# Optimization experiments

Hardware: AMD Instinct MI355X
Metric: run time of the kernel (lower is better)

Reference implementation:

```python
import jax, jax.numpy as jnp
import numpy as np

B, T, D, H = 2, 2048, 1024, 16
HD = D // H  # head_size = 64
EPS = 1e-5


def _layernorm(x, g, b):
    mu = jnp.mean(x, axis=-1, keepdims=True)
    var = jnp.mean(jnp.square(x - mu), axis=-1, keepdims=True)
    return (x - mu) * jax.lax.rsqrt(var + EPS) * g + b


def setup_inputs() -> dict:
    key = jax.random.key(0)
    ks = jax.random.split(key, 16)
    s = 0.02
    return {
        "x": jax.random.normal(ks[0], (B, T, D), jnp.float32),
        # per-head Q/K/V linears, stacked over heads: [H, D, HD] (in,out layout)
        "wq": jax.random.normal(ks[1], (H, D, HD), jnp.float32) * s,
        "bq": jnp.zeros((H, HD), jnp.float32),
        "wk": jax.random.normal(ks[2], (H, D, HD), jnp.float32) * s,
        "bk": jnp.zeros((H, HD), jnp.float32),
        "wv": jax.random.normal(ks[3], (H, D, HD), jnp.float32) * s,
        "bv": jnp.zeros((H, HD), jnp.float32),
        "wp": jax.random.normal(ks[4], (D, D), jnp.float32) * s,
        "bp": jnp.zeros((D,), jnp.float32),
        "w1": jax.random.normal(ks[5], (D, 4 * D), jnp.float32) * s,
        "b1": jnp.zeros((4 * D,), jnp.float32),
        "w2": jax.random.normal(ks[6], (4 * D, D), jnp.float32) * s,
        "b2": jnp.zeros((D,), jnp.float32),
        "ln1_g": jnp.ones((D,), jnp.float32),
        "ln1_b": jnp.zeros((D,), jnp.float32),
        "lnf_g": jnp.ones((D,), jnp.float32),
        "lnf_b": jnp.zeros((D,), jnp.float32),
        "ln2_g": jnp.ones((D,), jnp.float32),
        "ln2_b": jnp.zeros((D,), jnp.float32),
    }


def reference(x, wq, bq, wk, bk, wv, bv, wp, bp, w1, b1, w2, b2,
              ln1_g, ln1_b, lnf_g, lnf_b, ln2_g, ln2_b):
    b_, t_, d_ = x.shape
    # batched per-head projections: [B,H,T,HD]
    Q = jnp.einsum('btd,hde->bhte', x, wq) + bq[None, :, None, :]
    K = jnp.einsum('btd,hde->bhte', x, wk) + bk[None, :, None, :]
    V = jnp.einsum('btd,hde->bhte', x, wv) + bv[None, :, None, :]
    # raw attention scores, scaled -- NOTE: no softmax, no mask (matches source)
    wei = jnp.einsum('bhte,bhse->bhts', Q, K) * (HD ** -0.5)
    attn = jnp.einsum('bhts,bhse->bhte', wei, V)  # [B,H,T,HD]
    # concat heads along last dim == [B,T,H*HD]
    cat = attn.transpose(0, 2, 1, 3).reshape(b_, t_, d_)
    Kc = K.transpose(0, 2, 1, 3).reshape(b_, t_, d_)
    Vc = V.transpose(0, 2, 1, 3).reshape(b_, t_, d_)
    out = cat @ wp + bp
    out1 = _layernorm(x + out, ln1_g, ln1_b)
    # FeedForward: ln(idx + net(idx)) internally
    ff = jax.nn.relu(out1 @ w1 + b1) @ w2 + b2
    ffo = _layernorm(out1 + ff, lnf_g, lnf_b)
    out2 = _layernorm(out1 + ffo, ln2_g, ln2_b)
    return (out2, Kc, Vc)
```

## Files before the change

### kernel.cpp

```cpp
#include <hip/hip_runtime.h>

typedef unsigned short u16;
typedef __attribute__((ext_vector_type(4))) float f32x4;
typedef __attribute__((ext_vector_type(8))) __bf16 bf16x8;
typedef __attribute__((ext_vector_type(8))) unsigned short u16x8;
typedef __attribute__((ext_vector_type(4))) unsigned short u16x4;

__device__ __forceinline__ u16 f2b(float f) {
    unsigned int u = __builtin_bit_cast(unsigned int, f);
    u = (u + 0x7FFFu + ((u >> 16) & 1u)) >> 16;
    return (u16)u;
}
__device__ __forceinline__ float b2f(u16 h) {
    unsigned int u = ((unsigned int)h) << 16;
    return __builtin_bit_cast(float, u);
}

__device__ __forceinline__ void gload_lds16(const u16* g, u16* l) {
    __builtin_amdgcn_global_load_lds(
        (const __attribute__((address_space(1))) void*)g,
        (__attribute__((address_space(3))) void*)l,
        16, 0, 0);
}

__device__ __forceinline__ bf16x8 lds_frag(const u16* p) {
    u16x8 t = *(const u16x8*)p;
    return __builtin_bit_cast(bf16x8, t);
}

#define FENCE asm volatile("" ::: "memory")
#define BARRIER do { FENCE; __builtin_amdgcn_s_barrier(); FENCE; \
                     __builtin_amdgcn_sched_barrier(0); } while (0)
#define SCHED0 __builtin_amdgcn_sched_barrier(0)
#define LGKM0 do { asm volatile("s_waitcnt lgkmcnt(0)" ::: "memory"); \
                   __builtin_amdgcn_sched_barrier(0); } while (0)
#define WAIT_VM8 do { asm volatile("s_waitcnt vmcnt(8)" ::: "memory"); \
                      __builtin_amdgcn_sched_barrier(0); } while (0)
#define WAIT_VM0 do { asm volatile("s_waitcnt vmcnt(0)" ::: "memory"); \
                      __builtin_amdgcn_sched_barrier(0); } while (0)

__global__ __launch_bounds__(256) void cast_x_kernel(const float* __restrict__ in,
                                                     u16* __restrict__ out) {
    int i = (blockIdx.x * 256 + threadIdx.x) * 4;
    float4 v = *(const float4*)&in[i];
    u16x4 o = { f2b(v.x), f2b(v.y), f2b(v.z), f2b(v.w) };
    *(u16x4*)&out[i] = o;
}

__global__ __launch_bounds__(256) void tr_wqkv(const float* __restrict__ wq,
                                               const float* __restrict__ wk,
                                               const float* __restrict__ wv,
                                               u16* __restrict__ WT) {
    __shared__ float tile[32][33];
    int z = blockIdx.z;
    int sel = z >> 4, h = z & 15;
    const float* w = (sel == 0) ? wq : (sel == 1) ? wk : wv;
    w += (long)h * 65536;
    int tx = threadIdx.x & 31, ty = threadIdx.x >> 5;
    int d0 = blockIdx.x * 32, e0 = blockIdx.y * 32;
#pragma unroll
    for (int i = 0; i < 32; i += 8)
        tile[ty + i][tx] = w[(long)(d0 + ty + i) * 64 + e0 + tx];
    __syncthreads();
#pragma unroll
    for (int i = 0; i < 32; i += 8)
        WT[((long)(sel * 1024 + h * 64 + e0 + ty + i)) * 1024 + d0 + tx] = f2b(tile[tx][ty + i]);
}

__global__ __launch_bounds__(256) void prep_bias(const float* __restrict__ bq,
                                                 const float* __restrict__ bk,
                                                 const float* __restrict__ bv,
                                                 float* __restrict__ BI) {
    int i = blockIdx.x * 256 + threadIdx.x;
    const float* b = (i < 1024) ? bq : (i < 2048) ? bk : bv;
    BI[i] = b[((i & 1023) >> 6) * 64 + (i & 63)];
}

__global__ __launch_bounds__(256) void transpose_cast(const float* __restrict__ in,
                                                      u16* __restrict__ out, int R, int C) {
    __shared__ float tile[32][33];
    int tx = threadIdx.x & 31, ty = threadIdx.x >> 5;
    int r0 = blockIdx.y * 32, c0 = blockIdx.x * 32;
#pragma unroll
    for (int i = 0; i < 32; i += 8)
        tile[ty + i][tx] = in[(long)(r0 + ty + i) * C + c0 + tx];
    __syncthreads();
#pragma unroll
    for (int i = 0; i < 32; i += 8)
        out[(long)(c0 + ty + i) * R + r0 + tx] = f2b(tile[tx][ty + i]);
}

__global__ __launch_bounds__(256) void kv_expand(const u16* __restrict__ QKVB,
                                                 float* __restrict__ kv) {
    int idx = blockIdx.x * 256 + threadIdx.x;
    int row = idx >> 8;
    int co = (idx & 255) * 8;
    u16x8 v = *(const u16x8*)&QKVB[(long)row * 3072 + 1024 + co];
    float4 f0 = { b2f(v[0]), b2f(v[1]), b2f(v[2]), b2f(v[3]) };
    float4 f1 = { b2f(v[4]), b2f(v[5]), b2f(v[6]), b2f(v[7]) };
    long base = (long)(co >> 10) * 4194304 + (long)row * 1024 + (co & 1023);
    *(float4*)&kv[base] = f0;
    *(float4*)&kv[base + 4] = f1;
}

template <int MODE, int WM, int WN, int MF, int NF, bool COLOUT>
__global__ __launch_bounds__(WM * WN * 64, 2) void gemmT(
    const u16* __restrict__ A, const u16* __restrict__ BT, const float* __restrict__ bias,
    u16* __restrict__ Cb, u16* __restrict__ Q0, u16* __restrict__ Q1,
    int M, int N, int K, int lda, int ldb, int ldc, int kchunk) {
    constexpr int T   = WM * WN * 64;
    constexpr int BM  = WM * MF * 16;
    constexpr int BN  = WN * NF * 16;
    constexpr int RPI = T / 8;
    constexpr int LA  = BM / RPI;
    constexpr int LB  = BN / RPI;
    constexpr int EPI = T * 8;
    constexpr int MFH = MF / 2;
    constexpr int ASZ = BM * 64, BSZ = BN * 64;
    __shared__ __align__(16) u16 SMEM[2 * ASZ + 2 * BSZ];
    u16* As0 = SMEM;
    u16* As1 = SMEM + ASZ;
    u16* Bs0 = SMEM + 2 * ASZ;
    u16* Bs1 = SMEM + 2 * ASZ + BSZ;
    const int tid = threadIdx.x;
    const int lane = tid & 63;
    const int wid = tid >> 6;
    const int wr = wid / WN, wc = wid % WN;
    const int ntile = N / BN;
    const int mtile = M / BM;
    int bid = blockIdx.x;
    int kb = 0, ksz = K;
    u16* Pout = Q0;
    if (MODE == 4) {
        int tiles = mtile * ntile;
        int sk = bid / tiles; bid -= sk * tiles;
        kb = sk * kchunk;
        int rem = K - kb; ksz = rem < kchunk ? rem : kchunk;
        Pout = sk ? Q1 : Q0;
    }
    {
        int q = (mtile * ntile) >> 3;
        bid = (bid & 7) * q + (bid >> 3);
    }
    int bi, bj;
    if (COLOUT) { bj = bid / mtile; bi = bid % mtile; }
    else        { bi = bid / ntile; bj = bid % ntile; }
    const int brow = bi * BM, bcol = bj * BN;
    const int nt = ksz >> 6;

    const int srow = tid >> 3;
    const int scol = ((tid & 7) ^ (srow & 7)) << 3;
    const u16* ag = A + (long)(brow + srow) * lda + kb + scol;
    const u16* bg = BT + (long)(bcol + srow) * ldb + kb + scol;
    const long aI = (long)RPI * lda, bI = (long)RPI * ldb;
    const int sdst = tid << 3;

    auto STAGE = [&](u16* lA, u16* lB, int t) {
#pragma unroll
        for (int j = 0; j < LA; ++j)
            gload_lds16(ag + ((long)t << 6) + j * aI, &lA[j * EPI + sdst]);
#pragma unroll
        for (int j = 0; j < LB; ++j)
            gload_lds16(bg + ((long)t << 6) + j * bI, &lB[j * EPI + sdst]);
    };

    f32x4 acc[MF][NF] = {};
    bf16x8 af0[MFH], af1[MFH], bf0[NF], bf1[NF];

    const int ln15 = lane & 15;
    const int eoff = (((lane >> 4) << 3) ^ ((lane & 7) << 3));
    const int arow0 = wr * (MF * 16) + ln15;
    const int brow0 = wc * (NF * 16) + ln15;

#define RD_A(dst, S, kh, mh)                                                   \
    _Pragma("unroll") for (int m4 = 0; m4 < MFH; ++m4)                         \
        dst[m4] = lds_frag(&(S)[((arow0 + (((mh) * MFH + m4) << 4)) << 6) +    \
                                (eoff ^ ((kh) << 5))]);
#define RD_B(dst, S, kh)                                                       \
    _Pragma("unroll") for (int n = 0; n < NF; ++n)                             \
        dst[n] = lds_frag(&(S)[((brow0 + (n << 4)) << 6) + (eoff ^ ((kh) << 5))]);
#define MM(a, b, mh) do {                                                      \
    __builtin_amdgcn_s_setprio(1);                                             \
    _Pragma("unroll") for (int m4 = 0; m4 < MFH; ++m4)                         \
        _Pragma("unroll") for (int n = 0; n < NF; ++n)                         \
            acc[(mh) * MFH + m4][n] = __builtin_amdgcn_mfma_f32_16x16x32_bf16( \
                a[m4], b[n], acc[(mh) * MFH + m4][n], 0, 0, 0);                \
    __builtin_amdgcn_s_setprio(0);                                             \
} while (0)

    STAGE(As0, Bs0, 0);
    if (nt > 1) { STAGE(As1, Bs1, 1); WAIT_VM8; } else { WAIT_VM0; }
    BARRIER;
    RD_B(bf0, Bs0, 0);
    RD_A(af0, As0, 0, 0);

    u16 *Ac = As0, *Bc = Bs0, *Ao = As1, *Bo = Bs1;
    for (int t = 0; t < nt; ++t) {
        const bool hasN = (t + 1 < nt);
        const bool hasNN = (t + 2 < nt);
        RD_A(af1, Ac, 0, 1);
        MM(af0, bf0, 0);
        SCHED0;
        RD_B(bf1, Bc, 1);
        RD_A(af0, Ac, 1, 0);
        MM(af1, bf0, 1);
        SCHED0;
        RD_A(af1, Ac, 1, 1);
        MM(af0, bf1, 0);
        WAIT_VM0;
        BARRIER;
        if (hasN) { RD_B(bf0, Bo, 0); RD_A(af0, Ao, 0, 0); }
        MM(af1, bf1, 1);
        BARRIER;
        if (hasNN) STAGE(Ac, Bc, t + 2);
        SCHED0;
        u16* tp;
        tp = Ac; Ac = Ao; Ao = tp;
        tp = Bc; Bc = Bo; Bo = tp;
    }

    const int crow0 = wr * (MF * 16), ccol0 = wc * (NF * 16);
#pragma unroll
    for (int m = 0; m < MF; ++m) {
        int rbase = crow0 + (m << 4) + ((lane >> 4) << 2);
#pragma unroll
        for (int n = 0; n < NF; ++n) {
            int col = ccol0 + (n << 4) + ln15;
            float bv = (MODE == 4) ? 0.f : bias[bcol + col];
#pragma unroll
            for (int r = 0; r < 4; ++r) {
                float v = acc[m][n][r] + bv;
                if (MODE == 2) v = v > 0.f ? v : 0.f;
                int row = rbase + r;
                SMEM[row * BN + (col ^ ((row & 7) << 3))] = f2b(v);
            }
        }
    }
    LGKM0;
    BARRIER;
    u16* outp = (MODE == 4) ? Pout : Cb;
    constexpr int CHT = BM * BN / 8 / T;
#pragma unroll
    for (int k = 0; k < CHT; ++k) {
        int c = tid + k * T;
        int row = c / (BN / 8), co = (c % (BN / 8)) * 8;
        u16x8 vv = *(const u16x8*)&SMEM[row * BN + (co ^ ((row & 7) << 3))];
        *(u16x8*)&outp[(long)(brow + row) * ldc + bcol + co] = vv;
    }
#undef RD_A
#undef RD_B
#undef MM
}

__global__ __launch_bounds__(256) void ktv_partial(const u16* __restrict__ QKVB,
                                                   float* __restrict__ KTVF) {
    __shared__ __align__(16) u16 Ks[64 * 64];
    __shared__ __align__(16) u16 Vs[64 * 64];
    int tid = threadIdx.x;
    int tc = blockIdx.x, bh = blockIdx.y;
    int b = bh >> 4, h = bh & 15;
    int j = tid & 63, i0 = (tid >> 6) * 16;
    float acc[16] = {};
    for (int st = 0; st < 4; ++st) {
        int t0 = tc * 256 + st * 64;
        __syncthreads();
#pragma unroll
        for (int i = 0; i < 2; ++i) {
            int c = i * 256 + tid;
            long base = (long)(b * 2048 + t0 + (c >> 3)) * 3072 + h * 64 + (c & 7) * 8;
            *(u16x8*)&Ks[c * 8] = *(const u16x8*)&QKVB[base + 1024];
            *(u16x8*)&Vs[c * 8] = *(const u16x8*)&QKVB[base + 2048];
        }
        __syncthreads();
        for (int tt = 0; tt < 64; ++tt) {
            float vj = b2f(Vs[tt * 64 + j]);
            u16x8 k0 = *(const u16x8*)&Ks[tt * 64 + i0];
            u16x8 k1 = *(const u16x8*)&Ks[tt * 64 + i0 + 8];
#pragma unroll
            for (int r = 0; r < 8; ++r) acc[r] += b2f(k0[r]) * vj;
#pragma unroll
            for (int r = 0; r < 8; ++r) acc[r + 8] += b2f(k1[r]) * vj;
        }
    }
#pragma unroll
    for (int r = 0; r < 16; ++r)
        atomicAdd(&KTVF[bh * 4096 + (i0 + r) * 64 + j], acc[r]);
}

__global__ __launch_bounds__(256) void cast_ktv(const float* __restrict__ KTVF,
                                                u16* __restrict__ KTVT) {
    int idx = blockIdx.x * 256 + threadIdx.x;
    int bh = idx >> 12, r = idx & 4095;
    int n = r >> 6, k = r & 63;
    KTVT[idx] = f2b(KTVF[bh * 4096 + k * 64 + n] * 0.125f);
}

__global__ __launch_bounds__(256) void attn_gemm(const u16* __restrict__ QKVB,
                                                 const u16* __restrict__ KTVT,
                                                 u16* __restrict__ cat) {
    __shared__ __align__(16) u16 Qs[64 * 64];
    __shared__ __align__(16) u16 Bs[64 * 64];
    int tid = threadIdx.x, wid = tid >> 6, lane = tid & 63;
    int rt = blockIdx.x, bh = blockIdx.y;
    int b = bh >> 4, h = bh & 15;
    long qbase = (long)(b * 2048 + rt * 64) * 3072 + h * 64;
#pragma unroll
    for (int i = 0; i < 2; ++i) {
        int c = i * 256 + tid;
        gload_lds16(QKVB + qbase + (c >> 3) * 3072 + (c & 7) * 8, &Qs[(i * 256 + wid * 64) * 8]);
        gload_lds16(KTVT + bh * 4096 + c * 8, &Bs[(i * 256 + wid * 64) * 8]);
    }
    __syncthreads();
    f32x4 acc[4] = {};
#pragma unroll
    for (int kk = 0; kk < 2; ++kk) {
        bf16x8 a = lds_frag(&Qs[(wid * 16 + (lane & 15)) * 64 + kk * 32 + (lane >> 4) * 8]);
#pragma unroll
        for (int n = 0; n < 4; ++n) {
            bf16x8 bb = lds_frag(&Bs[(n * 16 + (lane & 15)) * 64 + kk * 32 + (lane >> 4) * 8]);
            acc[n] = __builtin_amdgcn_mfma_f32_16x16x32_bf16(a, bb, acc[n], 0, 0, 0);
        }
    }
#pragma unroll
    for (int n = 0; n < 4; ++n)
#pragma unroll
        for (int r = 0; r < 4; ++r) {
            int row = rt * 64 + wid * 16 + (lane >> 4) * 4 + r;
            int col = h * 64 + n * 16 + (lane & 15);
            cat[(long)(b * 2048 + row) * 1024 + col] = f2b(acc[n][r]);
        }
}

__device__ __forceinline__ void block_reduce2(float& a, float& b) {
    __syncthreads();
#pragma unroll
    for (int off = 32; off; off >>= 1) {
        a += __shfl_down(a, off);
        b += __shfl_down(b, off);
    }
    __shared__ float sa[4], sb[4];
    int wid = threadIdx.x >> 6, lane = threadIdx.x & 63;
    if (lane == 0) { sa[wid] = a; sb[wid] = b; }
    __syncthreads();
    a = sa[0] + sa[1] + sa[2] + sa[3];
    b = sb[0] + sb[1] + sb[2] + sb[3];
}

__global__ __launch_bounds__(256) void ln1_kernel(
    const float* __restrict__ x,
    const u16* __restrict__ q0, const u16* __restrict__ q1,
    const float* __restrict__ bp,
    const float* __restrict__ g, const float* __restrict__ bt,
    float* __restrict__ out1f, u16* __restrict__ out1b) {
    int row = blockIdx.x, tid = threadIdx.x;
    long base = (long)row * 1024 + tid * 4;
    float4 xv = *(const float4*)&x[base];
    u16x4 a0 = *(const u16x4*)&q0[base];
    u16x4 a1 = *(const u16x4*)&q1[base];
    float4 bb = *(const float4*)&bp[tid * 4];
    float xa[4] = { xv.x, xv.y, xv.z, xv.w };
    float bba[4] = { bb.x, bb.y, bb.z, bb.w };
    float s[4];
#pragma unroll
    for (int r = 0; r < 4; ++r)
        s[r] = xa[r] + b2f(a0[r]) + b2f(a1[r]) + bba[r];
    float sum = s[0] + s[1] + s[2] + s[3];
    float sq = s[0] * s[0] + s[1] * s[1] + s[2] * s[2] + s[3] * s[3];
    block_reduce2(sum, sq);
    float mu = sum * (1.f / 1024.f);
    float var = sq * (1.f / 1024.f) - mu * mu;
    float rs = rsqrtf(var + 1e-5f);
    float o0 = (s[0] - mu) * rs * g[tid * 4 + 0] + bt[tid * 4 + 0];
    float o1 = (s[1] - mu) * rs * g[tid * 4 + 1] + bt[tid * 4 + 1];
    float o2 = (s[2] - mu) * rs * g[tid * 4 + 2] + bt[tid * 4 + 2];
    float o3 = (s[3] - mu) * rs * g[tid * 4 + 3] + bt[tid * 4 + 3];
    float4 of; of.x = o0; of.y = o1; of.z = o2; of.w = o3;
    u16x4 ob = (u16x4){ f2b(o0), f2b(o1), f2b(o2), f2b(o3) };
    *(float4*)&out1f[base] = of;
    *(u16x4*)&out1b[base] = ob;
}

__global__ __launch_bounds__(256) void lnf_kernel(
    const float* __restrict__ out1f,
    const u16* __restrict__ q0, const u16* __restrict__ q1,
    const float* __restrict__ b2,
    const float* __restrict__ lnfg, const float* __restrict__ lnfb,
    const float* __restrict__ ln2g, const float* __restrict__ ln2b,
    float* __restrict__ out2) {
    int row = blockIdx.x, tid = threadIdx.x;
    long base = (long)row * 1024 + tid * 4;
    float4 o1 = *(const float4*)&out1f[base];
    u16x4 a0 = *(const u16x4*)&q0[base];
    u16x4 a1 = *(const u16x4*)&q1[base];
    float4 bb = *(const float4*)&b2[tid * 4];
    float o1a[4] = { o1.x, o1.y, o1.z, o1.w };
    float bba[4] = { bb.x, bb.y, bb.z, bb.w };
    float s1[4];
#pragma unroll
    for (int r = 0; r < 4; ++r)
        s1[r] = o1a[r] + b2f(a0[r]) + b2f(a1[r]) + bba[r];
    float sum = s1[0] + s1[1] + s1[2] + s1[3];
    float sq = s1[0] * s1[0] + s1[1] * s1[1] + s1[2] * s1[2] + s1[3] * s1[3];
    block_reduce2(sum, sq);
    float mu = sum * (1.f / 1024.f);
    float rs = rsqrtf(sq * (1.f / 1024.f) - mu * mu + 1e-5f);
    float s2[4];
#pragma unroll
    for (int r = 0; r < 4; ++r) {
        float ffo = (s1[r] - mu) * rs * lnfg[tid * 4 + r] + lnfb[tid * 4 + r];
        s2[r] = o1a[r] + ffo;
    }
    float sum2 = s2[0] + s2[1] + s2[2] + s2[3];
    float sq2 = s2[0] * s2[0] + s2[1] * s2[1] + s2[2] * s2[2] + s2[3] * s2[3];
    block_reduce2(sum2, sq2);
    float mu2 = sum2 * (1.f / 1024.f);
    float rs2 = rsqrtf(sq2 * (1.f / 1024.f) - mu2 * mu2 + 1e-5f);
    float4 o;
    o.x = (s2[0] - mu2) * rs2 * ln2g[tid * 4 + 0] + ln2b[tid * 4 + 0];
    o.y = (s2[1] - mu2) * rs2 * ln2g[tid * 4 + 1] + ln2b[tid * 4 + 1];
    o.z = (s2[2] - mu2) * rs2 * ln2g[tid * 4 + 2] + ln2b[tid * 4 + 2];
    o.w = (s2[3] - mu2) * rs2 * ln2g[tid * 4 + 3] + ln2b[tid * 4 + 3];
    *(float4*)&out2[base] = o;
}

extern "C" void kernel_launch(void* const* d_in, const int* in_sizes, int n_in,
                              void* d_out, int out_size, void* d_ws, size_t ws_size,
                              hipStream_t stream) {
    const float* x    = (const float*)d_in[0];
    const float* wq   = (const float*)d_in[1];
    const float* bq   = (const float*)d_in[2];
    const float* wk   = (const float*)d_in[3];
    const float* bk   = (const float*)d_in[4];
    const float* wv   = (const float*)d_in[5];
    const float* bv   = (const float*)d_in[6];
    const float* wp   = (const float*)d_in[7];
    const float* bp   = (const float*)d_in[8];
    const float* w1   = (const float*)d_in[9];
    const float* b1   = (const float*)d_in[10];
    const float* w2   = (const float*)d_in[11];
    const float* b2   = (const float*)d_in[12];
    const float* ln1g = (const float*)d_in[13];
    const float* ln1b = (const float*)d_in[14];
    const float* lnfg = (const float*)d_in[15];
    const float* lnfb = (const float*)d_in[16];
    const float* ln2g = (const float*)d_in[17];
    const float* ln2b = (const float*)d_in[18];

    float* out2 = (float*)d_out;
    float* kv   = (float*)d_out + 4194304;

    char* ws = (char*)d_ws;
    u16*   XB     = (u16*)  (ws + 0);
    u16*   CAT    = XB;
    u16*   WQKVT  = (u16*)  (ws + 8388608);
    float* BQKV   = (float*)(ws + 14680064);
    u16*   WPT    = (u16*)  (ws + 14692352);
    u16*   W1T    = (u16*)  (ws + 16789504);
    u16*   W2T    = (u16*)  (ws + 25178112);
    float* KTVF   = (float*)(ws + 33566720);
    u16*   KTVT   = (u16*)  (ws + 34091008);
    u16*   QKVB   = (u16*)  (ws + 34353152);
    u16*   OUT1B  = QKVB;
    u16*   Q3_0   = (u16*)  (ws + 59518976);
    u16*   Q3_1   = (u16*)  (ws + 67907584);
    float* OUT1F  = (float*)(ws + 76296192);
    u16*   H1     = (u16*)  (ws + 93073408);
    u16*   Q5_0   = (u16*)  (ws + 0);
    u16*   Q5_1   = (u16*)  (ws + 34353152);
    (void)ws_size; (void)in_sizes; (void)n_in; (void)out_size;

    hipMemsetAsync(KTVF, 0, 32 * 4096 * 4, stream);
    cast_x_kernel<<<4096, 256, 0, stream>>>(x, XB);
    tr_wqkv<<<dim3(32, 2, 48), 256, 0, stream>>>(wq, wk, wv, WQKVT);
    prep_bias<<<12, 256, 0, stream>>>(bq, bk, bv, BQKV);
    transpose_cast<<<dim3(32, 32), 256, 0, stream>>>(wp, WPT, 1024, 1024);
    transpose_cast<<<dim3(128, 32), 256, 0, stream>>>(w1, W1T, 1024, 4096);
    transpose_cast<<<dim3(32, 128), 256, 0, stream>>>(w2, W2T, 4096, 1024);

    gemmT<1, 2, 4, 4, 6, true><<<256, 512, 0, stream>>>(
        XB, WQKVT, BQKV, QKVB, nullptr, nullptr,
        4096, 3072, 1024, 1024, 1024, 3072, 0);
    kv_expand<<<4096, 256, 0, stream>>>(QKVB, kv);
    ktv_partial<<<dim3(8, 32), 256, 0, stream>>>(QKVB, KTVF);
    cast_ktv<<<512, 256, 0, stream>>>(KTVF, KTVT);
    attn_gemm<<<dim3(32, 32), 256, 0, stream>>>(QKVB, KTVT, CAT);

    gemmT<4, 2, 2, 4, 4, false><<<512, 256, 0, stream>>>(
        CAT, WPT, nullptr, nullptr, Q3_0, Q3_1,
        4096, 1024, 1024, 1024, 1024, 1024, 512);
    ln1_kernel<<<4096, 256, 0, stream>>>(x, Q3_0, Q3_1, bp, ln1g, ln1b, OUT1F, OUT1B);

    gemmT<2, 2, 4, 8, 4, false><<<256, 512, 0, stream>>>(
        OUT1B, W1T, b1, H1, nullptr, nullptr,
        4096, 4096, 1024, 1024, 1024, 4096, 0);
    gemmT<4, 2, 2, 4, 4, false><<<512, 256, 0, stream>>>(
        H1, W2T, nullptr, nullptr, Q5_0, Q5_1,
        4096, 1024, 4096, 4096, 4096, 1024, 2048);
    lnf_kernel<<<4096, 256, 0, stream>>>(OUT1F, Q5_0, Q5_1, b2,
                                         lnfg, lnfb, ln2g, ln2b, out2);
}
```

Measured before the change: 209.6 us.

## Fuse weight prep kernels, fold K/V fp32 expansion into QKV GEMM epilogue, retile FFN1

Merges the bias-prep and three transpose-cast launches into a single kernel that dispatches on block index, reducing launch count. The separate kv_expand pass is removed and the QKV GEMM epilogue now writes fp32 K/V outputs directly, which avoids re-reading the bf16 QKV buffer. The FFN1 GEMM moves from 512-thread 256x256-style tiles to smaller 256-thread tiles with 1024 blocks, trading per-block data reuse for better occupancy and load balance. The epilogue fusion adds extra global stores inside the GEMM's output loop.

New measurement: 207.6 us. Within noise of the previous version (-1.0%).

```diff
diff --git a/kernel.cpp b/kernel.cpp
--- a/kernel.cpp
+++ b/kernel.cpp
@@ -67,20 +67,25 @@
         WT[((long)(sel * 1024 + h * 64 + e0 + ty + i)) * 1024 + d0 + tx] = f2b(tile[tx][ty + i]);
 }
 
-__global__ __launch_bounds__(256) void prep_bias(const float* __restrict__ bq,
-                                                 const float* __restrict__ bk,
-                                                 const float* __restrict__ bv,
-                                                 float* __restrict__ BI) {
-    int i = blockIdx.x * 256 + threadIdx.x;
-    const float* b = (i < 1024) ? bq : (i < 2048) ? bk : bv;
-    BI[i] = b[((i & 1023) >> 6) * 64 + (i & 63)];
-}
-
-__global__ __launch_bounds__(256) void transpose_cast(const float* __restrict__ in,
-                                                      u16* __restrict__ out, int R, int C) {
+__global__ __launch_bounds__(256) void transpose_cast3(
+    const float* __restrict__ wp, const float* __restrict__ w1, const float* __restrict__ w2,
+    const float* __restrict__ bq, const float* __restrict__ bk, const float* __restrict__ bv,
+    u16* __restrict__ WPT, u16* __restrict__ W1T, u16* __restrict__ W2T,
+    float* __restrict__ BI) {
+    int bid = blockIdx.x;
+    if (bid >= 9216) {
+        int i = (bid - 9216) * 256 + threadIdx.x;
+        const float* b = (i < 1024) ? bq : (i < 2048) ? bk : bv;
+        BI[i] = b[((i & 1023) >> 6) * 64 + (i & 63)];
+        return;
+    }
+    const float* in; u16* out; int C, R, bx, by;
+    if (bid < 1024)      { in = wp; out = WPT; R = 1024; C = 1024; bx = bid & 31;  by = bid >> 5; }
+    else if (bid < 5120) { int b = bid - 1024; in = w1; out = W1T; R = 1024; C = 4096; bx = b & 127; by = b >> 7; }
+    else                 { int b = bid - 5120; in = w2; out = W2T; R = 4096; C = 1024; bx = b & 31;  by = b >> 5; }
     __shared__ float tile[32][33];
     int tx = threadIdx.x & 31, ty = threadIdx.x >> 5;
-    int r0 = blockIdx.y * 32, c0 = blockIdx.x * 32;
+    int r0 = by * 32, c0 = bx * 32;
 #pragma unroll
     for (int i = 0; i < 32; i += 8)
         tile[ty + i][tx] = in[(long)(r0 + ty + i) * C + c0 + tx];
@@ -90,23 +95,11 @@
         out[(long)(c0 + ty + i) * R + r0 + tx] = f2b(tile[tx][ty + i]);
 }
 
-__global__ __launch_bounds__(256) void kv_expand(const u16* __restrict__ QKVB,
-                                                 float* __restrict__ kv) {
-    int idx = blockIdx.x * 256 + threadIdx.x;
-    int row = idx >> 8;
-    int co = (idx & 255) * 8;
-    u16x8 v = *(const u16x8*)&QKVB[(long)row * 3072 + 1024 + co];
-    float4 f0 = { b2f(v[0]), b2f(v[1]), b2f(v[2]), b2f(v[3]) };
-    float4 f1 = { b2f(v[4]), b2f(v[5]), b2f(v[6]), b2f(v[7]) };
-    long base = (long)(co >> 10) * 4194304 + (long)row * 1024 + (co & 1023);
-    *(float4*)&kv[base] = f0;
-    *(float4*)&kv[base + 4] = f1;
-}
-
 template <int MODE, int WM, int WN, int MF, int NF, bool COLOUT>
 __global__ __launch_bounds__(WM * WN * 64, 2) void gemmT(
     const u16* __restrict__ A, const u16* __restrict__ BT, const float* __restrict__ bias,
-    u16* __restrict__ Cb, u16* __restrict__ Q0, u16* __restrict__ Q1,
+    u16* __restrict__ Cb, float* __restrict__ KV,
+    u16* __restrict__ Q0, u16* __restrict__ Q1,
     int M, int N, int K, int lda, int ldb, int ldc, int kchunk) {
     constexpr int T   = WM * WN * 64;
     constexpr int BM  = WM * MF * 16;
@@ -246,6 +239,17 @@
         int row = c / (BN / 8), co = (c % (BN / 8)) * 8;
         u16x8 vv = *(const u16x8*)&SMEM[row * BN + (co ^ ((row & 7) << 3))];
         *(u16x8*)&outp[(long)(brow + row) * ldc + bcol + co] = vv;
+        if (MODE == 1) {
+            int cg = bcol + co;
+            if (cg >= 1024) {
+                int cc = cg - 1024;
+                long kbase = (long)(cc >> 10) * 4194304 + (long)(brow + row) * 1024 + (cc & 1023);
+                float4 f0 = { b2f(vv[0]), b2f(vv[1]), b2f(vv[2]), b2f(vv[3]) };
+                float4 f1 = { b2f(vv[4]), b2f(vv[5]), b2f(vv[6]), b2f(vv[7]) };
+                *(float4*)&KV[kbase] = f0;
+                *(float4*)&KV[kbase + 4] = f1;
+            }
+        }
     }
 #undef RD_A
 #undef RD_B
@@ -472,29 +476,26 @@
     hipMemsetAsync(KTVF, 0, 32 * 4096 * 4, stream);
     cast_x_kernel<<<4096, 256, 0, stream>>>(x, XB);
     tr_wqkv<<<dim3(32, 2, 48), 256, 0, stream>>>(wq, wk, wv, WQKVT);
-    prep_bias<<<12, 256, 0, stream>>>(bq, bk, bv, BQKV);
-    transpose_cast<<<dim3(32, 32), 256, 0, stream>>>(wp, WPT, 1024, 1024);
-    transpose_cast<<<dim3(128, 32), 256, 0, stream>>>(w1, W1T, 1024, 4096);
-    transpose_cast<<<dim3(32, 128), 256, 0, stream>>>(w2, W2T, 4096, 1024);
+    transpose_cast3<<<9228, 256, 0, stream>>>(wp, w1, w2, bq, bk, bv,
+                                              WPT, W1T, W2T, BQKV);
 
     gemmT<1, 2, 4, 4, 6, true><<<256, 512, 0, stream>>>(
-        XB, WQKVT, BQKV, QKVB, nullptr, nullptr,
+        XB, WQKVT, BQKV, QKVB, kv, nullptr, nullptr,
         4096, 3072, 1024, 1024, 1024, 3072, 0);
-    kv_expand<<<4096, 256, 0, stream>>>(QKVB, kv);
     ktv_partial<<<dim3(8, 32), 256, 0, stream>>>(QKVB, KTVF);
     cast_ktv<<<512, 256, 0, stream>>>(KTVF, KTVT);
     attn_gemm<<<dim3(32, 32), 256, 0, stream>>>(QKVB, KTVT, CAT);
 
     gemmT<4, 2, 2, 4, 4, false><<<512, 256, 0, stream>>>(
-        CAT, WPT, nullptr, nullptr, Q3_0, Q3_1,
+        CAT, WPT, nullptr, nullptr, nullptr, Q3_0, Q3_1,
         4096, 1024, 1024, 1024, 1024, 1024, 512);
     ln1_kernel<<<4096, 256, 0, stream>>>(x, Q3_0, Q3_1, bp, ln1g, ln1b, OUT1F, OUT1B);
 
-    gemmT<2, 2, 4, 8, 4, false><<<256, 512, 0, stream>>>(
-        OUT1B, W1T, b1, H1, nullptr, nullptr,
+    gemmT<2, 2, 2, 4, 4, false><<<1024, 256, 0, stream>>>(
+        OUT1B, W1T, b1, H1, nullptr, nullptr, nullptr,
         4096, 4096, 1024, 1024, 1024, 4096, 0);
     gemmT<4, 2, 2, 4, 4, false><<<512, 256, 0, stream>>>(
-        H1, W2T, nullptr, nullptr, Q5_0, Q5_1,
+        H1, W2T, nullptr, nullptr, nullptr, Q5_0, Q5_1,
         4096, 1024, 4096, 4096, 4096, 1024, 2048);
     lnf_kernel<<<4096, 256, 0, stream>>>(OUT1F, Q5_0, Q5_1, b2,
                                          lnfg, lnfb, ln2g, ln2b, out2);
```
